# Kernel optimization log

Measured on AMD Instinct MI355X. Metric: run time of the kernel, lower is better.

## Reference

```python
import jax, jax.numpy as jnp
import numpy as np

N = 4096        # number of target nodes (also attention key length)
K = 10          # num_neighbors
E = 128         # embedding_dimension
EF = 64         # edge_feature_dim
T = 64          # time_encoding_dim
H = 2           # num_attention_heads
D = E + T       # query_dim = 192
KEY = E + EF + T            # per-neighbor key dim = 256
KD = KEY * K                # flattened kdim/vdim = 2560


def setup_inputs() -> dict:
    key = jax.random.key(0)
    ks = jax.random.split(key, 16)
    s = 0.02
    return {
        "features": jax.random.normal(ks[0], (N, E), jnp.float32),
        "edge_feats": jax.random.normal(ks[1], (N, K, EF), jnp.float32),
        "time_feats": jax.random.normal(ks[2], (N, K, T), jnp.float32),
        "neighbors": jax.random.randint(ks[3], (N, K), 0, N),
        "node_idx": jnp.arange(N),
        # MultiheadAttention projections (jax convention: x @ W + b, W is [in, out])
        "Wq": jax.random.normal(ks[4], (D, D), jnp.float32) * s,
        "bq": jnp.zeros((D,), jnp.float32),
        "Wk": jax.random.normal(ks[5], (KD, D), jnp.float32) * s,
        "bk": jnp.zeros((D,), jnp.float32),
        "Wv": jax.random.normal(ks[6], (KD, D), jnp.float32) * s,
        "bv": jnp.zeros((D,), jnp.float32),
        "Wo": jax.random.normal(ks[7], (D, D), jnp.float32) * s,
        "bo": jnp.zeros((D,), jnp.float32),
        # MLP([query_dim + embedding, embedding, embedding]) with ReLU between layers
        "W1": jax.random.normal(ks[8], (D + E, E), jnp.float32) * s,
        "b1": jnp.zeros((E,), jnp.float32),
        "W2": jax.random.normal(ks[9], (E, E), jnp.float32) * s,
        "b2": jnp.zeros((E,), jnp.float32),
    }


def reference(features, edge_feats, time_feats, neighbors, node_idx,
              Wq, bq, Wk, bk, Wv, bv, Wo, bo, W1, b1, W2, b2):
    n, k = neighbors.shape
    hd = D // H
    # _aggregate: gather neighbor node features, concat edge + time feats, flatten
    neigh = features[neighbors]                                       # [N, K, E]
    agg = jnp.concatenate([neigh, edge_feats, time_feats], axis=-1)   # [N, K, KEY]
    agg = agg.reshape(n, k * KEY)                                     # [N, KD]
    # query: node features padded with zero time encoding
    x = features[node_idx]                                            # [N, E]
    q_in = jnp.concatenate([x, jnp.zeros((n, T), features.dtype)], axis=-1)  # [N, D]
    # multi-head attention: batch=1, every query attends over all N aggregated keys
    q = (q_in @ Wq + bq).reshape(n, H, hd)
    kk = (agg @ Wk + bk).reshape(n, H, hd)
    vv = (agg @ Wv + bv).reshape(n, H, hd)
    scale = 1.0 / jnp.sqrt(jnp.asarray(hd, features.dtype))
    scores = jnp.einsum('nhd,mhd->hnm', q, kk) * scale                # [H, N, N]
    attn = jax.nn.softmax(scores, axis=-1)
    o = jnp.einsum('hnm,mhd->nhd', attn, vv).reshape(n, D)
    attn_out = o @ Wo + bo                                            # [N, D]
    # MLP over concat(node_feats, attn_out)
    h = jnp.concatenate([x, attn_out], axis=-1)                       # [N, D+E]
    return jax.nn.relu(h @ W1 + b1) @ W2 + b2                         # [N, E]
```

## Files before the change

### kernel.cpp

```cpp
#include <hip/hip_runtime.h>
#include <hip/hip_bf16.h>
#include <math.h>

#define NN   4096
#define KNB  10
#define ED   128
#define EFD  64
#define TD   64
#define DD   192
#define KEYD 256
#define KDD  2560
#define HD   96
#define NH   2
#define NSPLIT 4

typedef __attribute__((ext_vector_type(8))) short bf16x8;
typedef __attribute__((ext_vector_type(4))) float f32x4;
typedef __attribute__((ext_vector_type(2))) unsigned int u32x2;

__device__ inline short f2bf(float f) {
    union { float f; unsigned int u; } c; c.f = f;
    unsigned int r = (c.u + 0x7FFFu + ((c.u >> 16) & 1u)) >> 16;
    return (short)r;
}

__device__ inline float bf2f(short s) {
    union { unsigned int u; float f; } c;
    c.u = ((unsigned int)(unsigned short)s) << 16;
    return c.f;
}

__device__ inline void gload_lds16(const void* g, void* lds) {
    __builtin_amdgcn_global_load_lds(
        (const __attribute__((address_space(1))) void*)g,
        (__attribute__((address_space(3))) void*)lds, 16, 0, 0);
}

__global__ __launch_bounds__(256) void prep_convert(
    const float* __restrict__ Wk, const float* __restrict__ Wv,
    const float* __restrict__ Wq,
    const float* __restrict__ Wo, const float* __restrict__ bo,
    const float* __restrict__ W1, const float* __restrict__ b1,
    const float* __restrict__ W2,
    const float* __restrict__ features, const float* __restrict__ edge_feats,
    const float* __restrict__ time_feats, const int* __restrict__ node_idx,
    short* __restrict__ WkT, short* __restrict__ WvT, short* __restrict__ WqT,
    short* __restrict__ WcatT, short* __restrict__ W2T, float* __restrict__ bfold,
    short* __restrict__ featbf, short* __restrict__ xb,
    short* __restrict__ edgebf, short* __restrict__ timebf)
{
    int blk = blockIdx.x, t = threadIdx.x;
    if (blk < 254) {
        __shared__ float ts[64][65];
        const float* W; short* WT; int src_ld, dst_ld, k0, n0;
        if (blk < 240) {
            int z = blk / 120, r = blk % 120;
            W = z ? Wv : Wk; WT = z ? WvT : WkT;
            src_ld = DD; dst_ld = KDD; k0 = (r % 40) * 64; n0 = (r / 40) * 64;
        } else if (blk < 246) {
            int r = blk - 240;
            W = Wq; WT = WqT; src_ld = DD; dst_ld = ED;
            k0 = (r % 2) * 64; n0 = (r / 2) * 64;
        } else if (blk < 250) {
            int r = blk - 246;
            W = W1; WT = WcatT; src_ld = ED; dst_ld = 320;
            k0 = (r % 2) * 64; n0 = (r / 2) * 64;
        } else {
            int r = blk - 250;
            W = W2; WT = W2T; src_ld = ED; dst_ld = ED;
            k0 = (r % 2) * 64; n0 = (r / 2) * 64;
        }
        #pragma unroll
        for (int j = 0; j < 4; ++j) {
            int k = (t >> 4) + j * 16, n4 = (t & 15) * 4;
            float4 v = *(const float4*)&W[(size_t)(k0 + k) * src_ld + n0 + n4];
            ts[k][n4] = v.x; ts[k][n4 + 1] = v.y; ts[k][n4 + 2] = v.z; ts[k][n4 + 3] = v.w;
        }
        __syncthreads();
        int n = t >> 2, kc = (t & 3) * 16;
        short tmp[16];
        #pragma unroll
        for (int j = 0; j < 16; ++j) tmp[j] = f2bf(ts[kc + j][n]);
        *(bf16x8*)&WT[(size_t)(n0 + n) * dst_ld + k0 + kc] = *(bf16x8*)&tmp[0];
        *(bf16x8*)&WT[(size_t)(n0 + n) * dst_ld + k0 + kc + 8] = *(bf16x8*)&tmp[8];
    } else if (blk == 254) {
        if (t < 128) {
            float s = 0.f;
            for (int j = 0; j < DD; ++j) s += bo[j] * W1[(size_t)(ED + j) * ED + t];
            bfold[t] = s + b1[t];
        }
    } else if (blk < 447) {
        int d = blk - 255;
        if (t < 128) {
            float s = 0.f;
            for (int j = 0; j < DD; ++j)
                s += Wo[(size_t)d * DD + j] * W1[(size_t)(ED + j) * ED + t];
            WcatT[t * 320 + ED + d] = f2bf(s);
        }
    } else {
        int cb = blk - 447;
        if (cb < 512) {
            int e4 = cb * 256 + t;
            float4 v = *(const float4*)&features[(size_t)e4 * 4];
            short4 o; o.x = f2bf(v.x); o.y = f2bf(v.y); o.z = f2bf(v.z); o.w = f2bf(v.w);
            *(short4*)&featbf[(size_t)e4 * 4] = o;
        } else if (cb < 1024) {
            int l4 = (cb - 512) * 256 + t;
            int n = l4 >> 5, c = (l4 & 31) * 4;
            float4 v = *(const float4*)&features[(size_t)node_idx[n] * ED + c];
            short4 o; o.x = f2bf(v.x); o.y = f2bf(v.y); o.z = f2bf(v.z); o.w = f2bf(v.w);
            *(short4*)&xb[(size_t)n * ED + c] = o;
        } else if (cb < 3584) {
            int l4 = (cb - 1024) * 256 + t;
            float4 v = *(const float4*)&edge_feats[(size_t)l4 * 4];
            short4 o; o.x = f2bf(v.x); o.y = f2bf(v.y); o.z = f2bf(v.z); o.w = f2bf(v.w);
            *(short4*)&edgebf[(size_t)l4 * 4] = o;
        } else {
            int l4 = (cb - 3584) * 256 + t;
            float4 v = *(const float4*)&time_feats[(size_t)l4 * 4];
            short4 o; o.x = f2bf(v.x); o.y = f2bf(v.y); o.z = f2bf(v.z); o.w = f2bf(v.w);
            *(short4*)&timebf[(size_t)l4 * 4] = o;
        }
    }
}

__global__ __launch_bounds__(256) void kvq_gemm_mfma(
    const short* __restrict__ featbf, const short* __restrict__ edgebf,
    const short* __restrict__ timebf, const int* __restrict__ neighbors,
    const short* __restrict__ WkT, const short* __restrict__ WvT,
    short* __restrict__ psumK, short* __restrict__ psumV,
    const short* __restrict__ xb, const short* __restrict__ WqT,
    const float* __restrict__ bq, short* __restrict__ qb)
{
    __shared__ short As[2][128 * 64];
    __shared__ short Bs[2][64 * 64];
    __shared__ unsigned short nbr[128 * KNB];
    int tid = threadIdx.x, wid = tid >> 6, lane = tid & 63;
    int lx = lane & 15, lg = lane >> 4;
    int id = blockIdx.x;

    if (id < 768) {
        int xcd = id & 7, slot_ = id >> 3;
        int g = xcd * 16 + slot_ / 6;
        int nb = slot_ % 6;
        int mb = g >> 2, s = g & 3;
        bool isV = nb >= 3;
        const short* WT = isV ? WvT : WkT;
        int n0 = (nb - (isV ? 3 : 0)) * 64;
        int m0 = mb * 128;
        int wm0 = (wid >> 1) * 64, wn0 = (wid & 1) * 32;

        for (int i = tid; i < 128 * KNB; i += 256)
            nbr[i] = (unsigned short)neighbors[(size_t)m0 * KNB + i];
        __syncthreads();

        f32x4 acc[4][2] = {};

        auto stage = [&](int k0, int b) {
            #pragma unroll
            for (int it = 0; it < 4; ++it) {
                int idx = (wid * 4 + it) * 64 + lane;
                int m = idx >> 3, cs = (idx & 7) ^ (m & 7);
                int k = k0 + cs * 8;
                int slot = k >> 8, off = k & 255;
                int nbid = nbr[m * KNB + slot];
                const short* src;
                if (off < ED)
                    src = featbf + (size_t)nbid * ED + off;
                else if (off < ED + EFD)
                    src = edgebf + ((size_t)(m0 + m) * KNB + slot) * EFD + (off - ED);
                else
                    src = timebf + ((size_t)(m0 + m) * KNB + slot) * TD + (off - ED - EFD);
                gload_lds16(src, &As[b][(wid * 4 + it) * 512]);
            }
            #pragma unroll
            for (int it = 0; it < 2; ++it) {
                int idx = (wid * 2 + it) * 64 + lane;
                int n = idx >> 3, c = (idx & 7) ^ (n & 7);
                gload_lds16(WT + (size_t)(n0 + n) * KDD + k0 + c * 8,
                            &Bs[b][(wid * 2 + it) * 512]);
            }
        };

        int kbase = s * (KDD / NSPLIT);
        stage(kbase, 0);
        for (int i = 0; i < 10; ++i) {
            int b = i & 1;
            __syncthreads();
            if (i < 9) stage(kbase + (i + 1) * 64, b ^ 1);
            #pragma unroll
            for (int ks = 0; ks < 2; ++ks) {
                bf16x8 af[4], bfr[2];
                #pragma unroll
                for (int mf = 0; mf < 4; ++mf) {
                    int m = wm0 + mf * 16 + lx;
                    af[mf] = *(const bf16x8*)&As[b][m * 64 + (((ks * 4 + lg) ^ (m & 7)) << 3)];
                }
                #pragma unroll
                for (int nf = 0; nf < 2; ++nf) {
                    int n = wn0 + nf * 16 + lx;
                    bfr[nf] = *(const bf16x8*)&Bs[b][n * 64 + (((ks * 4 + lg) ^ (n & 7)) << 3)];
                }
                #pragma unroll
                for (int mf = 0; mf < 4; ++mf)
                    #pragma unroll
                    for (int nf = 0; nf < 2; ++nf)
                        acc[mf][nf] = __builtin_amdgcn_mfma_f32_16x16x32_bf16(
                            af[mf], bfr[nf], acc[mf][nf], 0, 0, 0);
            }
        }
        #pragma unroll
        for (int nf = 0; nf < 2; ++nf) {
            int ncol = n0 + wn0 + nf * 16 + lx;
            #pragma unroll
            for (int mf = 0; mf < 4; ++mf) {
                int mrow = m0 + wm0 + mf * 16 + 4 * lg;
                if (!isV) {
                    #pragma unroll
                    for (int r = 0; r < 4; ++r)
                        psumK[((size_t)s * NN + mrow + r) * DD + ncol] = f2bf(acc[mf][nf][r]);
                } else {
                    short4 s4;
                    s4.x = f2bf(acc[mf][nf][0]); s4.y = f2bf(acc[mf][nf][1]);
                    s4.z = f2bf(acc[mf][nf][2]); s4.w = f2bf(acc[mf][nf][3]);
                    *(short4*)&psumV[((size_t)(s * DD + ncol)) * NN + mrow] = s4;
                }
            }
        }
    } else {
        int qid = id - 768;
        int m0 = (qid / 3) * 64, n0 = (qid % 3) * 64;
        int wm0 = (wid >> 1) * 32, wn0 = (wid & 1) * 32;
        short* qAs = &As[0][0];
        short* qBs = &Bs[0][0];
        f32x4 acc[2][2] = {};

        for (int k0 = 0; k0 < ED; k0 += 64) {
            #pragma unroll
            for (int it = 0; it < 2; ++it) {
                int idx = (wid * 2 + it) * 64 + lane;
                int m = idx >> 3, c = (idx & 7) ^ (m & 7);
                gload_lds16(xb + (size_t)(m0 + m) * ED + k0 + c * 8, &qAs[(wid * 2 + it) * 512]);
            }
            #pragma unroll
            for (int it = 0; it < 2; ++it) {
                int idx = (wid * 2 + it) * 64 + lane;
                int n = idx >> 3, c = (idx & 7) ^ (n & 7);
                gload_lds16(WqT + (size_t)(n0 + n) * ED + k0 + c * 8, &qBs[(wid * 2 + it) * 512]);
            }
            __syncthreads();
            #pragma unroll
            for (int ks = 0; ks < 2; ++ks) {
                bf16x8 af[2], bfr[2];
                #pragma unroll
                for (int mf = 0; mf < 2; ++mf) {
                    int m = wm0 + mf * 16 + lx;
                    af[mf] = *(const bf16x8*)&qAs[m * 64 + (((ks * 4 + lg) ^ (m & 7)) << 3)];
                }
                #pragma unroll
                for (int nf = 0; nf < 2; ++nf) {
                    int n = wn0 + nf * 16 + lx;
                    bfr[nf] = *(const bf16x8*)&qBs[n * 64 + (((ks * 4 + lg) ^ (n & 7)) << 3)];
                }
                #pragma unroll
                for (int mf = 0; mf < 2; ++mf)
                    #pragma unroll
                    for (int nf = 0; nf < 2; ++nf)
                        acc[mf][nf] = __builtin_amdgcn_mfma_f32_16x16x32_bf16(
                            af[mf], bfr[nf], acc[mf][nf], 0, 0, 0);
            }
            __syncthreads();
        }
        const float scale = 0.10206207261596577f;
        #pragma unroll
        for (int nf = 0; nf < 2; ++nf) {
            int ncol = n0 + wn0 + nf * 16 + lx;
            float bb = bq[ncol];
            #pragma unroll
            for (int mf = 0; mf < 2; ++mf) {
                int mrow = m0 + wm0 + mf * 16 + 4 * lg;
                #pragma unroll
                for (int r = 0; r < 4; ++r)
                    qb[(size_t)(mrow + r) * DD + ncol] = f2bf((acc[mf][nf][r] + bb) * scale);
            }
        }
    }
}

__global__ __launch_bounds__(256) void kv_combine(
    const short* __restrict__ psumK, const short* __restrict__ psumV,
    const float* __restrict__ bk, const float* __restrict__ bv,
    short* __restrict__ kk, short* __restrict__ vvT)
{
    const int HALF = NN * DD / 4;
    int i = blockIdx.x * 256 + threadIdx.x;
    if (i < HALF) {
        int base = i * 4, n = base % DD;
        float sum[4] = {0.f, 0.f, 0.f, 0.f};
        #pragma unroll
        for (int s = 0; s < NSPLIT; ++s) {
            short4 v = *(const short4*)&psumK[(size_t)s * NN * DD + base];
            sum[0] += bf2f(v.x); sum[1] += bf2f(v.y);
            sum[2] += bf2f(v.z); sum[3] += bf2f(v.w);
        }
        float4 bb = *(const float4*)&bk[n];
        short4 o;
        o.x = f2bf(sum[0] + bb.x); o.y = f2bf(sum[1] + bb.y);
        o.z = f2bf(sum[2] + bb.z); o.w = f2bf(sum[3] + bb.w);
        *(short4*)&kk[base] = o;
    } else {
        int j = i - HALF;
        int base = j * 4, n = base / NN;
        float sum[4] = {0.f, 0.f, 0.f, 0.f};
        #pragma unroll
        for (int s = 0; s < NSPLIT; ++s) {
            short4 v = *(const short4*)&psumV[(size_t)s * DD * NN + base];
            sum[0] += bf2f(v.x); sum[1] += bf2f(v.y);
            sum[2] += bf2f(v.z); sum[3] += bf2f(v.w);
        }
        float bb = bv[n];
        short4 o;
        o.x = f2bf(sum[0] + bb); o.y = f2bf(sum[1] + bb);
        o.z = f2bf(sum[2] + bb); o.w = f2bf(sum[3] + bb);
        *(short4*)&vvT[base] = o;
    }
}

__global__ __launch_bounds__(512) void attn_mfma(
    const short* __restrict__ qb,
    const short* __restrict__ kk,
    const short* __restrict__ vvT,
    float* __restrict__ opart,
    float* __restrict__ ml)
{
    __shared__ short Ks[2][64 * 96];
    __shared__ short Vs[2][96 * 64];
    __shared__ short Ps[8][16 * 72];
    int tid = threadIdx.x, wid = tid >> 6, lane = tid & 63;
    int lx = lane & 15, lg = lane >> 4;
    int h = blockIdx.y, split = blockIdx.z;
    int hoff = h * HD;
    int qb0 = blockIdx.x * 128 + wid * 16;

    bf16x8 qf[3];
    #pragma unroll
    for (int ks = 0; ks < 3; ++ks)
        qf[ks] = *(const bf16x8*)&qb[(size_t)(qb0 + lx) * DD + hoff + ks * 32 + lg * 8];

    auto stage = [&](int kb, int b) {
        #pragma unroll
        for (int jj = 0; jj < 3; ++jj) {
            int j = wid * 3 + jj;
            if (j < 12) {
                int idx = j * 64 + lane;
                int row = idx / 12, c = idx % 12;
                gload_lds16(kk + (size_t)(kb + row) * DD + hoff + c * 8,
                            &Ks[b][j * 512]);
            } else {
                int idx = (j - 12) * 64 + lane;
                int d = idx >> 3, c = (idx & 7) ^ (d & 7);
                gload_lds16(vvT + (size_t)(hoff + d) * NN + kb + c * 8,
                            &Vs[b][(j - 12) * 512]);
            }
        }
    };

    float lsum = 0.0f;
    f32x4 accO[6] = {};
    short* myP = &Ps[wid][0];
    int kbase = split * (NN / NSPLIT);

    stage(kbase, 0);

    for (int t = 0; t < 16; ++t) {
        int b = t & 1;
        __syncthreads();
        f32x4 sf[4];
        #pragma unroll
        for (int nf = 0; nf < 4; ++nf) sf[nf] = (f32x4){0.f, 0.f, 0.f, 0.f};
        #pragma unroll
        for (int ks = 0; ks < 3; ++ks) {
            #pragma unroll
            for (int nf = 0; nf < 4; ++nf) {
                bf16x8 kf = *(const bf16x8*)&Ks[b][(nf * 16 + lx) * 96 + ks * 32 + lg * 8];
                sf[nf] = __builtin_amdgcn_mfma_f32_16x16x32_bf16(kf, qf[ks], sf[nf], 0, 0, 0);
            }
        }
        if (t < 15) stage(kbase + (t + 1) * 64, b ^ 1);
        #pragma unroll
        for (int nf = 0; nf < 4; ++nf) {
            float p0 = __expf(sf[nf][0]);
            float p1 = __expf(sf[nf][1]);
            float p2 = __expf(sf[nf][2]);
            float p3 = __expf(sf[nf][3]);
            lsum += (p0 + p1) + (p2 + p3);
            unsigned int u0, u1;
            asm("v_cvt_pk_bf16_f32 %0, %1, %2" : "=v"(u0) : "v"(p0), "v"(p1));
            asm("v_cvt_pk_bf16_f32 %0, %1, %2" : "=v"(u1) : "v"(p2), "v"(p3));
            *(u32x2*)&myP[lx * 72 + nf * 16 + 4 * lg] = (u32x2){u0, u1};
        }
        #pragma unroll
        for (int kf2 = 0; kf2 < 2; ++kf2) {
            bf16x8 pf = *(const bf16x8*)&myP[lx * 72 + kf2 * 32 + lg * 8];
            #pragma unroll
            for (int nf2 = 0; nf2 < 6; ++nf2) {
                int d = nf2 * 16 + lx;
                bf16x8 vf = *(const bf16x8*)&Vs[b][d * 64 + (((kf2 * 4 + lg) ^ (d & 7)) << 3)];
                accO[nf2] = __builtin_amdgcn_mfma_f32_16x16x32_bf16(pf, vf, accO[nf2], 0, 0, 0);
            }
        }
    }

    float* op = opart + ((size_t)split * NN + qb0) * DD + hoff;
    #pragma unroll
    for (int nf2 = 0; nf2 < 6; ++nf2)
        #pragma unroll
        for (int r = 0; r < 4; ++r)
            op[(size_t)(4 * lg + r) * DD + nf2 * 16 + lx] = accO[nf2][r];
    lsum += __shfl_xor(lsum, 16);
    lsum += __shfl_xor(lsum, 32);
    if (lane < 16)
        ml[((size_t)(split * NH + h)) * NN + qb0 + lx] = lsum;
}

__global__ __launch_bounds__(256) void mlp_fused(
    const short* __restrict__ xb,
    const float* __restrict__ opart,
    const float* __restrict__ ml,
    const short* __restrict__ WcatT,
    const float* __restrict__ bfold,
    const short* __restrict__ W2T,
    const float* __restrict__ b2,
    float* __restrict__ out)
{
    __shared__ short As[16 * 64];
    __shared__ short Bs[128 * 64];
    __shared__ short Ts[16 * 128];
    __shared__ float linv[32];
    int tid = threadIdx.x, wid = tid >> 6, lane = tid & 63;
    int lx = lane & 15, lg = lane >> 4;
    int m0 = blockIdx.x * 16;
    int wn0 = wid * 32;

    if (tid < 32) {
        int rl = tid >> 1, hh = tid & 1;
        float l = 0.f;
        #pragma unroll
        for (int s = 0; s < NSPLIT; ++s) l += ml[(size_t)(s * NH + hh) * NN + m0 + rl];
        linv[tid] = 1.0f / l;
    }

    f32x4 acc[2] = {};
    for (int step = 0; step < 5; ++step) {
        int k0 = step * 64;
        if (step < 2) {
            if (wid < 2) {
                int idx = tid;
                int m = idx >> 3, c = (idx & 7) ^ (m & 7);
                gload_lds16(xb + (size_t)(m0 + m) * ED + k0 + c * 8, &As[wid * 512]);
            }
        } else {
            if (tid < 128) {
                int m = tid >> 3, j8 = tid & 7;
                int dg = (k0 - 128) + j8 * 8;
                float sum[8];
                float4 a0 = *(const float4*)&opart[((size_t)0 * NN + m0 + m) * DD + dg];
                float4 a1 = *(const float4*)&opart[((size_t)0 * NN + m0 + m) * DD + dg + 4];
                sum[0] = a0.x; sum[1] = a0.y; sum[2] = a0.z; sum[3] = a0.w;
                sum[4] = a1.x; sum[5] = a1.y; sum[6] = a1.z; sum[7] = a1.w;
                #pragma unroll
                for (int s = 1; s < NSPLIT; ++s) {
                    float4 b0 = *(const float4*)&opart[((size_t)s * NN + m0 + m) * DD + dg];
                    float4 b1v = *(const float4*)&opart[((size_t)s * NN + m0 + m) * DD + dg + 4];
                    sum[0] += b0.x; sum[1] += b0.y; sum[2] += b0.z; sum[3] += b0.w;
                    sum[4] += b1v.x; sum[5] += b1v.y; sum[6] += b1v.z; sum[7] += b1v.w;
                }
                float inv = linv[m * 2 + (dg >= HD ? 1 : 0)];
                short tmp[8];
                #pragma unroll
                for (int j = 0; j < 8; ++j) tmp[j] = f2bf(sum[j] * inv);
                *(bf16x8*)&As[m * 64 + ((j8 ^ (m & 7)) << 3)] = *(bf16x8*)&tmp[0];
            }
        }
        #pragma unroll
        for (int it = 0; it < 4; ++it) {
            int idx = (wid * 4 + it) * 64 + lane;
            int n = idx >> 3, c = (idx & 7) ^ (n & 7);
            gload_lds16(WcatT + (size_t)n * 320 + k0 + c * 8, &Bs[(wid * 4 + it) * 512]);
        }
        __syncthreads();
        #pragma unroll
        for (int kss = 0; kss < 2; ++kss) {
            int m = lx;
            bf16x8 af = *(const bf16x8*)&As[m * 64 + (((kss * 4 + lg) ^ (m & 7)) << 3)];
            #pragma unroll
            for (int nf = 0; nf < 2; ++nf) {
                int n = wn0 + nf * 16 + lx;
                bf16x8 bfr = *(const bf16x8*)&Bs[n * 64 + (((kss * 4 + lg) ^ (n & 7)) << 3)];
                acc[nf] = __builtin_amdgcn_mfma_f32_16x16x32_bf16(af, bfr, acc[nf], 0, 0, 0);
            }
        }
        __syncthreads();
    }
    #pragma unroll
    for (int nf = 0; nf < 2; ++nf) {
        int kcol = wn0 + nf * 16 + lx;
        float bb = bfold[kcol];
        #pragma unroll
        for (int r = 0; r < 4; ++r) {
            int m = 4 * lg + r;
            float v = fmaxf(acc[nf][r] + bb, 0.f);
            Ts[m * 128 + ((((kcol >> 3) ^ (m & 7)) << 3) | (kcol & 7))] = f2bf(v);
        }
    }
    __syncthreads();
    f32x4 acc2[2] = {};
    #pragma unroll
    for (int step = 0; step < 2; ++step) {
        int k0 = step * 64;
        #pragma unroll
        for (int it = 0; it < 4; ++it) {
            int idx = (wid * 4 + it) * 64 + lane;
            int n = idx >> 3, c = (idx & 7) ^ (n & 7);
            gload_lds16(W2T + (size_t)n * 128 + k0 + c * 8, &Bs[(wid * 4 + it) * 512]);
        }
        __syncthreads();
        #pragma unroll
        for (int kss = 0; kss < 2; ++kss) {
            int m = lx;
            int chunk = step * 8 + kss * 4 + lg;
            bf16x8 af = *(const bf16x8*)&Ts[m * 128 + ((chunk ^ (m & 7)) << 3)];
            #pragma unroll
            for (int nf = 0; nf < 2; ++nf) {
                int n = wn0 + nf * 16 + lx;
                bf16x8 bfr = *(const bf16x8*)&Bs[n * 64 + (((kss * 4 + lg) ^ (n & 7)) << 3)];
                acc2[nf] = __builtin_amdgcn_mfma_f32_16x16x32_bf16(af, bfr, acc2[nf], 0, 0, 0);
            }
        }
        __syncthreads();
    }
    #pragma unroll
    for (int nf = 0; nf < 2; ++nf) {
        int ncol = wn0 + nf * 16 + lx;
        float bb = b2[ncol];
        #pragma unroll
        for (int r = 0; r < 4; ++r)
            out[(size_t)(m0 + 4 * lg + r) * 128 + ncol] = acc2[nf][r] + bb;
    }
}

extern "C" void kernel_launch(void* const* d_in, const int* in_sizes, int n_in,
                              void* d_out, int out_size, void* d_ws, size_t ws_size,
                              hipStream_t stream) {
    const float* features   = (const float*)d_in[0];
    const float* edge_feats = (const float*)d_in[1];
    const float* time_feats = (const float*)d_in[2];
    const int*   neighbors  = (const int*)d_in[3];
    const int*   node_idx   = (const int*)d_in[4];
    const float* Wq = (const float*)d_in[5];
    const float* bq = (const float*)d_in[6];
    const float* Wk = (const float*)d_in[7];
    const float* bk = (const float*)d_in[8];
    const float* Wv = (const float*)d_in[9];
    const float* bv = (const float*)d_in[10];
    const float* Wo = (const float*)d_in[11];
    const float* bo = (const float*)d_in[12];
    const float* W1 = (const float*)d_in[13];
    const float* b1 = (const float*)d_in[14];
    const float* W2 = (const float*)d_in[15];
    const float* b2 = (const float*)d_in[16];
    float* out = (float*)d_out;

    char* w = (char*)d_ws;
    short* featbf = (short*)w;  w += (size_t)NN * ED * 2;
    short* xb     = (short*)w;  w += (size_t)NN * ED * 2;
    short* edgebf = (short*)w;  w += (size_t)NN * KNB * EFD * 2;
    short* timebf = (short*)w;  w += (size_t)NN * KNB * TD * 2;
    short* qb     = (short*)w;  w += (size_t)NN * DD * 2;
    short* kkb    = (short*)w;  w += (size_t)NN * DD * 2;
    short* vvT    = (short*)w;  w += (size_t)DD * NN * 2;
    short* WkT    = (short*)w;  w += (size_t)DD * KDD * 2;
    short* WvT    = (short*)w;  w += (size_t)DD * KDD * 2;
    short* WqT    = (short*)w;  w += (size_t)DD * ED * 2;
    short* WcatT  = (short*)w;  w += (size_t)ED * 320 * 2;
    short* W2T    = (short*)w;  w += (size_t)ED * ED * 2;
    float* bfold  = (float*)w;  w += (size_t)ED * 4;
    short* psumK = (short*)w;
    short* psumV = psumK + (size_t)NSPLIT * NN * DD;
    float* opart = (float*)w;
    float* ml    = opart + (size_t)NSPLIT * NN * DD;

    prep_convert<<<6591, 256, 0, stream>>>(
        Wk, Wv, Wq, Wo, bo, W1, b1, W2,
        features, edge_feats, time_feats, node_idx,
        WkT, WvT, WqT, WcatT, W2T, bfold, featbf, xb, edgebf, timebf);
    kvq_gemm_mfma<<<6 * (NN / 128) * NSPLIT + 192, 256, 0, stream>>>(
        featbf, edgebf, timebf, neighbors, WkT, WvT, psumK, psumV, xb, WqT, bq, qb);
    kv_combine<<<2 * NN * DD / 4 / 256, 256, 0, stream>>>(psumK, psumV, bk, bv, kkb, vvT);
    attn_mfma<<<dim3(NN / 128, NH, NSPLIT), 512, 0, stream>>>(qb, kkb, vvT, opart, ml);
    mlp_fused<<<NN / 16, 256, 0, stream>>>(xb, opart, ml, WcatT, bfold, W2T, b2, out);
}
```

Before: 71.35 us.

## Fuse K and V projection tiles to share gathered A tile, reorder attention prefetch

Each KV GEMM block now computes both the K and V projections for the same row and column tile, so the gathered neighbor A tile is loaded once and used for two sets of MFMAs. This halves the KV block count and the redundant gather traffic. The cost is doubled accumulator registers and more LDS for the two B tiles. Separately, the attention kernel now issues its next-tile prefetch before the QK MFMAs instead of after them, to overlap loads with more compute.

```diff
diff --git a/kernel.cpp b/kernel.cpp
--- a/kernel.cpp
+++ b/kernel.cpp
@@ -133,20 +133,18 @@
     const float* __restrict__ bq, short* __restrict__ qb)
 {
     __shared__ short As[2][128 * 64];
-    __shared__ short Bs[2][64 * 64];
+    __shared__ short Bs[2][2][64 * 64];
     __shared__ unsigned short nbr[128 * KNB];
     int tid = threadIdx.x, wid = tid >> 6, lane = tid & 63;
     int lx = lane & 15, lg = lane >> 4;
     int id = blockIdx.x;
 
-    if (id < 768) {
+    if (id < 384) {
         int xcd = id & 7, slot_ = id >> 3;
-        int g = xcd * 16 + slot_ / 6;
-        int nb = slot_ % 6;
+        int g = xcd * 16 + slot_ / 3;
+        int nb = slot_ % 3;
         int mb = g >> 2, s = g & 3;
-        bool isV = nb >= 3;
-        const short* WT = isV ? WvT : WkT;
-        int n0 = (nb - (isV ? 3 : 0)) * 64;
+        int n0 = nb * 64;
         int m0 = mb * 128;
         int wm0 = (wid >> 1) * 64, wn0 = (wid & 1) * 32;
 
@@ -154,7 +152,7 @@
             nbr[i] = (unsigned short)neighbors[(size_t)m0 * KNB + i];
         __syncthreads();
 
-        f32x4 acc[4][2] = {};
+        f32x4 accK[4][2] = {}, accV[4][2] = {};
 
         auto stage = [&](int k0, int b) {
             #pragma unroll
@@ -177,8 +175,15 @@
             for (int it = 0; it < 2; ++it) {
                 int idx = (wid * 2 + it) * 64 + lane;
                 int n = idx >> 3, c = (idx & 7) ^ (n & 7);
-                gload_lds16(WT + (size_t)(n0 + n) * KDD + k0 + c * 8,
-                            &Bs[b][(wid * 2 + it) * 512]);
+                gload_lds16(WkT + (size_t)(n0 + n) * KDD + k0 + c * 8,
+                            &Bs[b][0][(wid * 2 + it) * 512]);
+            }
+            #pragma unroll
+            for (int it = 0; it < 2; ++it) {
+                int idx = (wid * 2 + it) * 64 + lane;
+                int n = idx >> 3, c = (idx & 7) ^ (n & 7);
+                gload_lds16(WvT + (size_t)(n0 + n) * KDD + k0 + c * 8,
+                            &Bs[b][1][(wid * 2 + it) * 512]);
             }
         };
 
@@ -190,7 +195,7 @@
             if (i < 9) stage(kbase + (i + 1) * 64, b ^ 1);
             #pragma unroll
             for (int ks = 0; ks < 2; ++ks) {
-                bf16x8 af[4], bfr[2];
+                bf16x8 af[4], bk8[2], bv8[2];
                 #pragma unroll
                 for (int mf = 0; mf < 4; ++mf) {
                     int m = wm0 + mf * 16 + lx;
@@ -199,14 +204,19 @@
                 #pragma unroll
                 for (int nf = 0; nf < 2; ++nf) {
                     int n = wn0 + nf * 16 + lx;
-                    bfr[nf] = *(const bf16x8*)&Bs[b][n * 64 + (((ks * 4 + lg) ^ (n & 7)) << 3)];
+                    int o = n * 64 + (((ks * 4 + lg) ^ (n & 7)) << 3);
+                    bk8[nf] = *(const bf16x8*)&Bs[b][0][o];
+                    bv8[nf] = *(const bf16x8*)&Bs[b][1][o];
                 }
                 #pragma unroll
                 for (int mf = 0; mf < 4; ++mf)
                     #pragma unroll
-                    for (int nf = 0; nf < 2; ++nf)
-                        acc[mf][nf] = __builtin_amdgcn_mfma_f32_16x16x32_bf16(
-                            af[mf], bfr[nf], acc[mf][nf], 0, 0, 0);
+                    for (int nf = 0; nf < 2; ++nf) {
+                        accK[mf][nf] = __builtin_amdgcn_mfma_f32_16x16x32_bf16(
+                            af[mf], bk8[nf], accK[mf][nf], 0, 0, 0);
+                        accV[mf][nf] = __builtin_amdgcn_mfma_f32_16x16x32_bf16(
+                            af[mf], bv8[nf], accV[mf][nf], 0, 0, 0);
+                    }
             }
         }
         #pragma unroll
@@ -215,24 +225,21 @@
             #pragma unroll
             for (int mf = 0; mf < 4; ++mf) {
                 int mrow = m0 + wm0 + mf * 16 + 4 * lg;
-                if (!isV) {
-                    #pragma unroll
-                    for (int r = 0; r < 4; ++r)
-                        psumK[((size_t)s * NN + mrow + r) * DD + ncol] = f2bf(acc[mf][nf][r]);
-                } else {
-                    short4 s4;
-                    s4.x = f2bf(acc[mf][nf][0]); s4.y = f2bf(acc[mf][nf][1]);
-                    s4.z = f2bf(acc[mf][nf][2]); s4.w = f2bf(acc[mf][nf][3]);
-                    *(short4*)&psumV[((size_t)(s * DD + ncol)) * NN + mrow] = s4;
-                }
+                #pragma unroll
+                for (int r = 0; r < 4; ++r)
+                    psumK[((size_t)s * NN + mrow + r) * DD + ncol] = f2bf(accK[mf][nf][r]);
+                short4 s4;
+                s4.x = f2bf(accV[mf][nf][0]); s4.y = f2bf(accV[mf][nf][1]);
+                s4.z = f2bf(accV[mf][nf][2]); s4.w = f2bf(accV[mf][nf][3]);
+                *(short4*)&psumV[((size_t)(s * DD + ncol)) * NN + mrow] = s4;
             }
         }
     } else {
-        int qid = id - 768;
+        int qid = id - 384;
         int m0 = (qid / 3) * 64, n0 = (qid % 3) * 64;
         int wm0 = (wid >> 1) * 32, wn0 = (wid & 1) * 32;
         short* qAs = &As[0][0];
-        short* qBs = &Bs[0][0];
+        short* qBs = &Bs[0][0][0];
         f32x4 acc[2][2] = {};
 
         for (int k0 = 0; k0 < ED; k0 += 64) {
@@ -375,6 +382,7 @@
     for (int t = 0; t < 16; ++t) {
         int b = t & 1;
         __syncthreads();
+        if (t < 15) stage(kbase + (t + 1) * 64, b ^ 1);
         f32x4 sf[4];
         #pragma unroll
         for (int nf = 0; nf < 4; ++nf) sf[nf] = (f32x4){0.f, 0.f, 0.f, 0.f};
@@ -386,7 +394,6 @@
                 sf[nf] = __builtin_amdgcn_mfma_f32_16x16x32_bf16(kf, qf[ks], sf[nf], 0, 0, 0);
             }
         }
-        if (t < 15) stage(kbase + (t + 1) * 64, b ^ 1);
         #pragma unroll
         for (int nf = 0; nf < 4; ++nf) {
             float p0 = __expf(sf[nf][0]);
@@ -594,7 +601,7 @@
         Wk, Wv, Wq, Wo, bo, W1, b1, W2,
         features, edge_feats, time_feats, node_idx,
         WkT, WvT, WqT, WcatT, W2T, bfold, featbf, xb, edgebf, timebf);
-    kvq_gemm_mfma<<<6 * (NN / 128) * NSPLIT + 192, 256, 0, stream>>>(
+    kvq_gemm_mfma<<<384 + 192, 256, 0, stream>>>(
         featbf, edgebf, timebf, neighbors, WkT, WvT, psumK, psumV, xb, WqT, bq, qb);
     kv_combine<<<2 * NN * DD / 4 / 256, 256, 0, stream>>>(psumK, psumV, bk, bv, kkb, vvT);
     attn_mfma<<<dim3(NN / 128, NH, NSPLIT), 512, 0, stream>>>(qb, kkb, vvT, opart, ml);
```

After: 69.63 us. 2.4% less time.
